# Performance work log

Measured on AMD Instinct MI355X. Metric: run time of the kernel, lower is better.

## Reference

```python
import jax, jax.numpy as jnp
import numpy as np

B, S, D = 4, 2048, 1024
H, HD = 16, 64
TAU = HD ** -0.5
N_MASKED = 256  # last keys masked (padding)


def setup_inputs() -> dict:
    key = jax.random.key(0)
    ks = jax.random.split(key, 8)
    sc = 0.02
    mask = jnp.zeros((B, 1, 1, S), dtype=bool).at[..., S - N_MASKED:].set(True)
    return {
        "q": jax.random.normal(ks[0], (B, S, D), dtype=jnp.float32),
        "k": jax.random.normal(ks[1], (B, S, D), dtype=jnp.float32),
        "v": jax.random.normal(ks[2], (B, S, D), dtype=jnp.float32),
        "mask": mask,
        "Wq": jax.random.normal(ks[3], (D, H * HD), dtype=jnp.float32) * sc,
        "bq": jnp.zeros((H * HD,), dtype=jnp.float32),
        "Wk": jax.random.normal(ks[4], (D, H * HD), dtype=jnp.float32) * sc,
        "bk": jnp.zeros((H * HD,), dtype=jnp.float32),
        "Wv": jax.random.normal(ks[5], (D, H * HD), dtype=jnp.float32) * sc,
        "bv": jnp.zeros((H * HD,), dtype=jnp.float32),
        "Wo": jax.random.normal(ks[6], (H * HD, D), dtype=jnp.float32) * sc,
        "bo": jnp.zeros((D,), dtype=jnp.float32),
    }


def reference(q, k, v, mask, Wq, bq, Wk, bk, Wv, bv, Wo, bo):
    # projections: [..., s, D] -> [..., s, H, HD]
    qh = (q @ Wq + bq).reshape(*q.shape[:-1], H, HD)
    kh = (k @ Wk + bk).reshape(*k.shape[:-1], H, HD)
    vh = (v @ Wv + bv).reshape(*v.shape[:-1], H, HD)
    # scores: [B, H, Q, K]
    attn = jnp.einsum('bqhd,bkhd->bhqk', qh, kh) * TAU
    attn = jnp.where(mask, -jnp.inf, attn)  # masked_fill(mask, -inf)
    # dropout(p=0) before softmax is identity
    p = jax.nn.softmax(attn, axis=-1)
    out = jnp.einsum('bhqk,bkhd->bqhd', p, vh).reshape(*q.shape[:-1], H * HD)
    return out @ Wo + bo  # [B, S, D]
```

## Files before the change

kernel.cpp:

```cpp
#include <hip/hip_runtime.h>
#include <hip/hip_fp16.h>
#include <cstdint>
#include <cstddef>

#define B_  4
#define S_  2048
#define D_  1024
#define H_  16
#define HD_ 64
#define TAU_ 0.125f
#define QSCALE_ 0.18033688011112042f

typedef _Float16 f16;
typedef __attribute__((ext_vector_type(8)))  _Float16 f16x8;
typedef __attribute__((ext_vector_type(4)))  _Float16 f16x4;
typedef __attribute__((ext_vector_type(2)))  __fp16   fp16x2_b;
typedef __attribute__((ext_vector_type(4)))  float    f32x4;
typedef __attribute__((ext_vector_type(16))) float    f32x16;
typedef __attribute__((ext_vector_type(2)))  unsigned u32x2;

__device__ __forceinline__ void gload_lds16(const void* g, void* l) {
    __builtin_amdgcn_global_load_lds(
        (const __attribute__((address_space(1))) unsigned int*)g,
        (__attribute__((address_space(3)))       unsigned int*)l,
        16, 0, 0);
}

__device__ __forceinline__ unsigned pkh(float a, float b) {
    fp16x2_b h = __builtin_amdgcn_cvt_pkrtz(a, b);
    return __builtin_bit_cast(unsigned, h);
}

__device__ __forceinline__ float exp2_hw(float x) {
    float r;
    asm("v_exp_f32 %0, %1" : "=v"(r) : "v"(x));
    return r;
}

__device__ __forceinline__ float max3f(float a, float b, float c) {
    float r;
    asm("v_max3_f32 %0, %1, %2, %3" : "=v"(r) : "v"(a), "v"(b), "v"(c));
    return r;
}

__device__ __forceinline__ float pair_max(float x) {
    unsigned xu = __builtin_bit_cast(unsigned, x);
    u32x2 r = __builtin_amdgcn_permlane32_swap(xu, xu, false, false);
    return fmaxf(__builtin_bit_cast(float, r[0]), __builtin_bit_cast(float, r[1]));
}
__device__ __forceinline__ float pair_sum(float x) {
    unsigned xu = __builtin_bit_cast(unsigned, x);
    u32x2 r = __builtin_amdgcn_permlane32_swap(xu, xu, false, false);
    return __builtin_bit_cast(float, r[0]) + __builtin_bit_cast(float, r[1]);
}

__global__ __launch_bounds__(256) void mask_norm_kernel(
    const unsigned char* __restrict__ mp, unsigned char* __restrict__ nm,
    float* __restrict__ mf)
{
    __shared__ int flags[3];
    const int tid = threadIdx.x;
    if (tid < 3) flags[tid] = 0;
    __syncthreads();
    int loc0 = 0, loc1 = 0, loc2 = 0;
    for (int i = 0; i < 32; ++i) {
        int off = tid * 32 + i;
        unsigned char v = mp[off];
        if (v) {
            int m = off & 3;
            if (m == 0) loc0 = 1;
            else if (m == 1) loc1 = 1;
            else loc2 = 1;
        }
    }
    if (loc0) atomicOr(&flags[0], 1);
    if (loc1) atomicOr(&flags[1], 1);
    if (loc2) atomicOr(&flags[2], 1);
    __syncthreads();
    const int mode = flags[1] ? 0 : (flags[2] ? 2 : (flags[0] ? 1 : 0));
    for (int i = 0; i < 32; ++i) {
        int idx = tid * 32 + i;
        unsigned char r;
        if (mode == 0)      r = mp[idx] ? 1 : 0;
        else if (mode == 1) r = ((const int*)mp)[idx] ? 1 : 0;
        else                r = (((const float*)mp)[idx] != 0.f) ? 1 : 0;
        nm[idx] = r;
        mf[idx] = r ? -1e30f : 0.f;
    }
}

__global__ __launch_bounds__(256) void wconv_kernel(
    const float* __restrict__ W0, const float* __restrict__ W1,
    const float* __restrict__ W2, const float* __restrict__ W3,
    f16* __restrict__ Wt)
{
    __shared__ float T[64][65];
    const int z = blockIdx.z;
    const float* W = (z == 0) ? W0 : (z == 1) ? W1 : (z == 2) ? W2 : W3;
    f16* out = Wt + (size_t)z * D_ * D_;
    const int n0 = blockIdx.x * 64, k0 = blockIdx.y * 64;
    const int tid = threadIdx.x;
    for (int j = 0; j < 4; ++j) {
        int idx = j * 256 + tid;
        int r = idx >> 4, c4 = idx & 15;
        float4 v = *(const float4*)&W[(size_t)(k0 + r) * D_ + n0 + c4 * 4];
        T[r][c4 * 4 + 0] = v.x; T[r][c4 * 4 + 1] = v.y;
        T[r][c4 * 4 + 2] = v.z; T[r][c4 * 4 + 3] = v.w;
    }
    __syncthreads();
    for (int j = 0; j < 16; ++j) {
        int idx = j * 256 + tid;
        int nl = idx >> 6, kl = idx & 63;
        out[(size_t)(n0 + nl) * D_ + k0 + kl] = (f16)T[kl][nl];
    }
}

__global__ __launch_bounds__(256) void gemm_qkvf_kernel(
    const float* __restrict__ q, const float* __restrict__ k,
    const float* __restrict__ v, const f16* __restrict__ Wt,
    const float* __restrict__ bq, const float* __restrict__ bk,
    const float* __restrict__ bv, f16* __restrict__ outbase)
{
    __shared__ __align__(16) float Al[128 * 64];
    __shared__ __align__(16) f16  Bl[128 * 64];
    const int z = blockIdx.z;
    const float* A  = (z == 0) ? q  : (z == 1) ? k  : v;
    const float* bi = (z == 0) ? bq : (z == 1) ? bk : bv;
    const f16*  W   = Wt + (size_t)z * D_ * D_;
    f16* Cp         = outbase + (size_t)z * S_ * B_ * D_;
    const float oscale = (z == 0) ? QSCALE_ : 1.f;
    const int outmode  = (z == 2) ? 1 : 0;
    const int m0 = blockIdx.x * 128, n0 = blockIdx.y * 128;
    const int tid = threadIdx.x, lane = tid & 63, wid = tid >> 6;
    const int wm = (wid >> 1) * 64, wn = (wid & 1) * 64;
    const int g = lane >> 4, c = lane & 15;

    f32x4 acc[4][4] = {};

    for (int kt = 0; kt < 16; ++kt) {
        const int k0 = kt * 64;
        for (int i = 0; i < 4; ++i) {
            int ch  = wid * 4 + i;
            int row = ch * 8 + (lane >> 3);
            int ls  = (lane & 7) ^ (row & 7);
            gload_lds16(W + (size_t)(n0 + row) * 1024 + k0 + ls * 8,
                        Bl + ch * 512);
        }
        for (int i = 0; i < 8; ++i) {
            int ch  = wid * 8 + i;
            int row = ch * 4 + (lane >> 4);
            int ls  = (lane & 15) ^ (row & 15);
            gload_lds16(A + (size_t)(m0 + row) * 1024 + k0 + ls * 4,
                        Al + ch * 256);
        }
        __syncthreads();
        for (int kc = 0; kc < 2; ++kc) {
            f16x8 af[4], bf[4];
            for (int mb = 0; mb < 4; ++mb) {
                int row = wm + mb * 16 + c;
                int sl  = kc * 8 + g * 2;
                f32x4 a0 = *(const f32x4*)&Al[row * 64 + ((sl)     ^ (row & 15)) * 4];
                f32x4 a1 = *(const f32x4*)&Al[row * 64 + ((sl + 1) ^ (row & 15)) * 4];
                f16x8 hfr;
                hfr[0] = (f16)a0[0]; hfr[1] = (f16)a0[1];
                hfr[2] = (f16)a0[2]; hfr[3] = (f16)a0[3];
                hfr[4] = (f16)a1[0]; hfr[5] = (f16)a1[1];
                hfr[6] = (f16)a1[2]; hfr[7] = (f16)a1[3];
                af[mb] = hfr;
            }
            for (int nb = 0; nb < 4; ++nb) {
                int row = wn + nb * 16 + c;
                bf[nb] = *(const f16x8*)&Bl[row * 64 + ((kc * 4 + g) ^ (row & 7)) * 8];
            }
            for (int mb = 0; mb < 4; ++mb)
                for (int nb = 0; nb < 4; ++nb)
                    acc[mb][nb] = __builtin_amdgcn_mfma_f32_16x16x32_f16(
                        af[mb], bf[nb], acc[mb][nb], 0, 0, 0);
        }
        __syncthreads();
    }
    for (int nb = 0; nb < 4; ++nb) {
        int n = n0 + wn + nb * 16 + c;
        float bv2 = bi[n];
        for (int mb = 0; mb < 4; ++mb)
            for (int r = 0; r < 4; ++r) {
                int m = m0 + wm + mb * 16 + g * 4 + r;
                float val = (acc[mb][nb][r] + bv2) * oscale;
                if (outmode == 1) {
                    Cp[(((size_t)(m >> 11) * H_ + (n >> 6)) * HD_ + (n & 63)) * S_ + (m & 2047)] = (f16)val;
                } else {
                    Cp[(size_t)m * 1024 + n] = (f16)val;
                }
            }
    }
}

__global__ __launch_bounds__(256) void gemm_out_kernel(
    const f16* __restrict__ Oh, const f16* __restrict__ WtO,
    const float* __restrict__ bo, float* __restrict__ out)
{
    __shared__ __align__(16) f16 Al[128 * 64];
    __shared__ __align__(16) f16 Bl[128 * 64];
    const int m0 = blockIdx.x * 128, n0 = blockIdx.y * 128;
    const int tid = threadIdx.x, lane = tid & 63, wid = tid >> 6;
    const int wm = (wid >> 1) * 64, wn = (wid & 1) * 64;
    const int g = lane >> 4, c = lane & 15;

    f32x4 acc[4][4] = {};

    for (int kt = 0; kt < 16; ++kt) {
        const int k0 = kt * 64;
        for (int i = 0; i < 4; ++i) {
            int ch  = wid * 4 + i;
            int row = ch * 8 + (lane >> 3);
            int ls  = (lane & 7) ^ (row & 7);
            gload_lds16(WtO + (size_t)(n0 + row) * 1024 + k0 + ls * 8,
                        Bl + ch * 512);
            gload_lds16(Oh + (size_t)(m0 + row) * 1024 + k0 + ls * 8,
                        Al + ch * 512);
        }
        __syncthreads();
        for (int kc = 0; kc < 2; ++kc) {
            f16x8 af[4], bf[4];
            for (int mb = 0; mb < 4; ++mb) {
                int row = wm + mb * 16 + c;
                af[mb] = *(const f16x8*)&Al[row * 64 + ((kc * 4 + g) ^ (row & 7)) * 8];
            }
            for (int nb = 0; nb < 4; ++nb) {
                int row = wn + nb * 16 + c;
                bf[nb] = *(const f16x8*)&Bl[row * 64 + ((kc * 4 + g) ^ (row & 7)) * 8];
            }
            for (int mb = 0; mb < 4; ++mb)
                for (int nb = 0; nb < 4; ++nb)
                    acc[mb][nb] = __builtin_amdgcn_mfma_f32_16x16x32_f16(
                        af[mb], bf[nb], acc[mb][nb], 0, 0, 0);
        }
        __syncthreads();
    }
    for (int nb = 0; nb < 4; ++nb) {
        int n = n0 + wn + nb * 16 + c;
        float bv = bo[n];
        for (int mb = 0; mb < 4; ++mb)
            for (int r = 0; r < 4; ++r) {
                int m = m0 + wm + mb * 16 + g * 4 + r;
                out[(size_t)m * 1024 + n] = acc[mb][nb][r] + bv;
            }
    }
}

__global__ __launch_bounds__(256, 2) void attn_kernel(
    const f16* __restrict__ qh, const f16* __restrict__ kh,
    const f16* __restrict__ vt, const unsigned char* __restrict__ maskp,
    const float* __restrict__ maskf, f16* __restrict__ Oh)
{
    __shared__ __align__(16) f16 Kl[2][128 * 64];
    __shared__ __align__(16) f16 VTl[2][64 * 128];
    const int tid = threadIdx.x, lane = tid & 63, wid = tid >> 6;
    const int ql = lane & 31, hi = lane >> 5;
    const int lg = ((blockIdx.x & 7) << 7) + (blockIdx.x >> 3);
    const int h = (lg >> 4) & 15, b = lg >> 8;
    const int q0 = (lg & 15) * 128 + wid * 32;

    const unsigned char* mrow = maskp + (size_t)b * S_;
    const float* mfrow = maskf + (size_t)b * S_;
    const size_t kbase  = (size_t)b * S_ * D_ + (size_t)h * HD_;
    const size_t vtbase = ((size_t)b * H_ + h) * (size_t)HD_ * S_;

    unsigned live = 0, part = 0;
    for (int t = 0; t < 16; ++t) {
        unsigned long long b0 = __ballot(mrow[t * 128 + lane] != 0);
        unsigned long long b1 = __ballot(mrow[t * 128 + 64 + lane] != 0);
        if (b0 != ~0ull || b1 != ~0ull) {
            live |= 1u << t;
            if (b0 | b1) part |= 1u << t;
        }
    }

    f16x8 qf[4];
    {
        const f16* qrow = qh + ((size_t)(b * S_ + q0 + ql) * H_ + h) * HD_;
        #pragma unroll
        for (int dc = 0; dc < 4; ++dc)
            qf[dc] = *(const f16x8*)&qrow[dc * 16 + hi * 8];
    }

    float m_ = -1e30f, l_ = 0.f;
    f32x16 accO[2] = {};

    auto stage = [&](int kv0, int bb) {
        #pragma unroll
        for (int i = 0; i < 4; ++i) {
            int ch  = wid * 4 + i;
            int row = ch * 8 + (lane >> 3);
            int ls  = (lane & 7) ^ (row & 7);
            gload_lds16(kh + kbase + (size_t)(kv0 + row) * D_ + ls * 8,
                        &Kl[bb][ch * 512]);
            int hdr = ch * 4 + (lane >> 4);
            int vs  = (lane & 15) ^ (hdr & 15);
            gload_lds16(vt + vtbase + (size_t)hdr * S_ + kv0 + vs * 8,
                        &VTl[bb][ch * 512]);
        }
    };

    if (live) {
        int t = __builtin_ctz(live);
        stage(t * 128, 0);
        __syncthreads();
        int cur = 0;
        for (;;) {
            unsigned rem = live & (0xFFFFFFFEu << t);
            int tn = rem ? __builtin_ctz(rem) : 32;
            if (tn < 32) stage(tn * 128, cur ^ 1);

            const int kv0 = t * 128;
            const f16* Kb = &Kl[cur][0];
            const f16* Vb = &VTl[cur][0];

            f32x16 sacc[4] = {};
            __builtin_amdgcn_s_setprio(1);
            #pragma unroll
            for (int ks = 0; ks < 4; ++ks) {
                const int key = ks * 32 + ql;
                #pragma unroll
                for (int dc = 0; dc < 4; ++dc) {
                    int slot = (dc * 2 + hi) ^ (key & 7);
                    f16x8 kf = *(const f16x8*)&Kb[key * 64 + slot * 8];
                    sacc[ks] = __builtin_amdgcn_mfma_f32_32x32x16_f16(
                        kf, qf[dc], sacc[ks], 0, 0, 0);
                }
            }
            __builtin_amdgcn_s_setprio(0);
            if (part & (1u << t)) {
                #pragma unroll
                for (int ks = 0; ks < 4; ++ks)
                    #pragma unroll
                    for (int r = 0; r < 16; ++r) {
                        int key = kv0 + ks * 32 + (r & 3) + 8 * (r >> 2) + 4 * hi;
                        sacc[ks][r] += mfrow[key];
                    }
            }
            float mx;
            {
                float m0 = max3f(sacc[0][0], sacc[0][1], sacc[0][2]);
                float m1 = max3f(sacc[1][0], sacc[1][1], sacc[1][2]);
                float m2 = max3f(sacc[2][0], sacc[2][1], sacc[2][2]);
                float m3 = max3f(sacc[3][0], sacc[3][1], sacc[3][2]);
                #pragma unroll
                for (int r = 3; r < 15; r += 2) {
                    m0 = max3f(m0, sacc[0][r], sacc[0][r + 1]);
                    m1 = max3f(m1, sacc[1][r], sacc[1][r + 1]);
                    m2 = max3f(m2, sacc[2][r], sacc[2][r + 1]);
                    m3 = max3f(m3, sacc[3][r], sacc[3][r + 1]);
                }
                m0 = fmaxf(m0, sacc[0][15]); m1 = fmaxf(m1, sacc[1][15]);
                m2 = fmaxf(m2, sacc[2][15]); m3 = fmaxf(m3, sacc[3][15]);
                mx = max3f(m0, m1, m2);
                mx = fmaxf(mx, m3);
            }
            mx = pair_max(mx);
            if (__ballot(mx > m_ + 8.f)) {
                float mnew = fmaxf(m_, mx);
                float alpha = exp2_hw(m_ - mnew);
                m_ = mnew;
                l_ *= alpha;
                #pragma unroll
                for (int blk = 0; blk < 2; ++blk)
                    #pragma unroll
                    for (int r = 0; r < 16; ++r) accO[blk][r] *= alpha;
            }
            float ts = 0.f;
            #pragma unroll
            for (int ks = 0; ks < 4; ++ks)
                #pragma unroll
                for (int r = 0; r < 16; ++r) {
                    float p = exp2_hw(sacc[ks][r] - m_);
                    sacc[ks][r] = p;
                    ts += p;
                }
            l_ += pair_sum(ts);

            #pragma unroll
            for (int ks = 0; ks < 4; ++ks) {
                unsigned Pq[4][2];
                #pragma unroll
                for (int j = 0; j < 4; ++j) {
                    Pq[j][0] = pkh(sacc[ks][4 * j + 0], sacc[ks][4 * j + 1]);
                    Pq[j][1] = pkh(sacc[ks][4 * j + 2], sacc[ks][4 * j + 3]);
                }
                #pragma unroll
                for (int kc = 0; kc < 2; ++kc) {
                    union { f16x8 v; unsigned u[4]; } pf;
                    u32x2 s0 = __builtin_amdgcn_permlane32_swap(Pq[2 * kc][0], Pq[2 * kc + 1][0], false, false);
                    u32x2 s1 = __builtin_amdgcn_permlane32_swap(Pq[2 * kc][1], Pq[2 * kc + 1][1], false, false);
                    pf.u[0] = s0[0]; pf.u[2] = s0[1];
                    pf.u[1] = s1[0]; pf.u[3] = s1[1];
                    const int s = ks * 2 + kc;
                    __builtin_amdgcn_s_setprio(1);
                    #pragma unroll
                    for (int blk = 0; blk < 2; ++blk) {
                        int hd = blk * 32 + ql;
                        int slot = (s * 2 + hi) ^ (hd & 15);
                        f16x8 vtf = *(const f16x8*)&Vb[hd * 128 + slot * 8];
                        accO[blk] = __builtin_amdgcn_mfma_f32_32x32x16_f16(
                            vtf, pf.v, accO[blk], 0, 0, 0);
                    }
                    __builtin_amdgcn_s_setprio(0);
                }
            }
            __syncthreads();
            cur ^= 1;
            if (tn == 32) break;
            t = tn;
        }
    }
    const float invl = (l_ > 0.f) ? 1.f / l_ : 0.f;
    f16* orow = Oh + ((size_t)(b * S_ + q0 + ql) * H_ + h) * HD_;
    #pragma unroll
    for (int blk = 0; blk < 2; ++blk)
        #pragma unroll
        for (int j = 0; j < 4; ++j) {
            f16x4 o;
            #pragma unroll
            for (int tt = 0; tt < 4; ++tt)
                o[tt] = (f16)(accO[blk][4 * j + tt] * invl);
            *(f16x4*)&orow[blk * 32 + 4 * hi + 8 * j] = o;
        }
}

extern "C" void kernel_launch(void* const* d_in, const int* in_sizes, int n_in,
                              void* d_out, int out_size, void* d_ws, size_t ws_size,
                              hipStream_t stream)
{
    const float* q    = (const float*)d_in[0];
    const float* k    = (const float*)d_in[1];
    const float* v    = (const float*)d_in[2];
    const unsigned char* mask = (const unsigned char*)d_in[3];
    const float* Wq   = (const float*)d_in[4];
    const float* bq   = (const float*)d_in[5];
    const float* Wk   = (const float*)d_in[6];
    const float* bk   = (const float*)d_in[7];
    const float* Wv   = (const float*)d_in[8];
    const float* bv   = (const float*)d_in[9];
    const float* Wo   = (const float*)d_in[10];
    const float* bo   = (const float*)d_in[11];
    float* out        = (float*)d_out;

    char* ws = (char*)d_ws;
    const size_t MB = 1048576;
    f16* Wt  = (f16*)ws;
    f16* qh  = (f16*)(ws + 8 * MB);
    f16* khp = (f16*)(ws + 24 * MB);
    f16* vtp = (f16*)(ws + 40 * MB);
    f16* Ohp = (f16*)(ws + 56 * MB);
    unsigned char* nm = (unsigned char*)(ws + 72 * MB);
    float* mf = (float*)(ws + 72 * MB + 8192);

    mask_norm_kernel<<<1, 256, 0, stream>>>(mask, nm, mf);
    wconv_kernel<<<dim3(16, 16, 4), 256, 0, stream>>>(Wq, Wk, Wv, Wo, Wt);
    gemm_qkvf_kernel<<<dim3(64, 8, 3), 256, 0, stream>>>(q, k, v, Wt, bq, bk, bv, qh);
    attn_kernel<<<1024, 256, 0, stream>>>(qh, khp, vtp, nm, mf, Ohp);
    gemm_out_kernel<<<dim3(64, 8), 256, 0, stream>>>(Ohp, Wt + (size_t)3 * D_ * D_, bo, out);
}
```

Measured before the change: 230.9 us.

## Pre-convert QKV inputs to fp16 and double-buffer projection GEMMs

Adds a pass that converts the fp32 q/k/v activations to fp16 in workspace, so the QKV projection GEMM can use async global-to-LDS loads with a double-buffered prefetch of the next K tile. The output projection GEMM gets the same double-buffering and both raise MFMA wave priority around the compute. The cost is an extra read-write pass over the activations and more LDS per block. The new path runs only when the workspace is large enough.

```diff
diff --git a/kernel.cpp b/kernel.cpp
--- a/kernel.cpp
+++ b/kernel.cpp
@@ -112,6 +112,106 @@
         int idx = j * 256 + tid;
         int nl = idx >> 6, kl = idx & 63;
         out[(size_t)(n0 + nl) * D_ + k0 + kl] = (f16)T[kl][nl];
+    }
+}
+
+__global__ __launch_bounds__(256) void f32to16_kernel(
+    const float* __restrict__ a0, const float* __restrict__ a1,
+    const float* __restrict__ a2, f16* __restrict__ o0,
+    f16* __restrict__ o1, f16* __restrict__ o2)
+{
+    const int z = blockIdx.y;
+    const float* a = (z == 0) ? a0 : (z == 1) ? a1 : a2;
+    f16* o = (z == 0) ? o0 : (z == 1) ? o1 : o2;
+    const int N4 = (B_ * S_ * D_) / 4;
+    for (int i = blockIdx.x * 256 + threadIdx.x; i < N4; i += gridDim.x * 256) {
+        float4 v = ((const float4*)a)[i];
+        f16x4 h;
+        h[0] = (f16)v.x; h[1] = (f16)v.y; h[2] = (f16)v.z; h[3] = (f16)v.w;
+        ((f16x4*)o)[i] = h;
+    }
+}
+
+__global__ __launch_bounds__(256, 2) void gemm_qkv16_kernel(
+    const f16* __restrict__ qf16, const f16* __restrict__ kf16,
+    const f16* __restrict__ vf16, const f16* __restrict__ Wt,
+    const float* __restrict__ bq, const float* __restrict__ bk,
+    const float* __restrict__ bv, f16* __restrict__ outbase)
+{
+    __shared__ __align__(16) f16 Al[2][128 * 64];
+    __shared__ __align__(16) f16 Bl[2][128 * 64];
+    const int z = blockIdx.z;
+    const f16* A    = (z == 0) ? qf16 : (z == 1) ? kf16 : vf16;
+    const float* bi = (z == 0) ? bq : (z == 1) ? bk : bv;
+    const f16*  W   = Wt + (size_t)z * D_ * D_;
+    f16* Cp         = outbase + (size_t)z * S_ * B_ * D_;
+    const float oscale = (z == 0) ? QSCALE_ : 1.f;
+    const int outmode  = (z == 2) ? 1 : 0;
+    const int m0 = blockIdx.x * 128, n0 = blockIdx.y * 128;
+    const int tid = threadIdx.x, lane = tid & 63, wid = tid >> 6;
+    const int wm = (wid >> 1) * 64, wn = (wid & 1) * 64;
+    const int g = lane >> 4, c = lane & 15;
+
+    f32x4 acc[4][4] = {};
+
+    auto stage = [&](int kt, int bb) {
+        const int k0 = kt * 64;
+        #pragma unroll
+        for (int i = 0; i < 4; ++i) {
+            int ch  = wid * 4 + i;
+            int row = ch * 8 + (lane >> 3);
+            int ls  = (lane & 7) ^ (row & 7);
+            gload_lds16(W + (size_t)(n0 + row) * 1024 + k0 + ls * 8,
+                        &Bl[bb][ch * 512]);
+            gload_lds16(A + (size_t)(m0 + row) * 1024 + k0 + ls * 8,
+                        &Al[bb][ch * 512]);
+        }
+    };
+
+    stage(0, 0);
+    __syncthreads();
+    int cur = 0;
+    for (int kt = 0; kt < 16; ++kt) {
+        if (kt < 15) stage(kt + 1, cur ^ 1);
+        #pragma unroll
+        for (int kc = 0; kc < 2; ++kc) {
+            f16x8 af[4], bf[4];
+            #pragma unroll
+            for (int mb = 0; mb < 4; ++mb) {
+                int row = wm + mb * 16 + c;
+                af[mb] = *(const f16x8*)&Al[cur][row * 64 + ((kc * 4 + g) ^ (row & 7)) * 8];
+            }
+            #pragma unroll
+            for (int nb = 0; nb < 4; ++nb) {
+                int row = wn + nb * 16 + c;
+                bf[nb] = *(const f16x8*)&Bl[cur][row * 64 + ((kc * 4 + g) ^ (row & 7)) * 8];
+            }
+            __builtin_amdgcn_s_setprio(1);
+            #pragma unroll
+            for (int mb = 0; mb < 4; ++mb)
+                #pragma unroll
+                for (int nb = 0; nb < 4; ++nb)
+                    acc[mb][nb] = __builtin_amdgcn_mfma_f32_16x16x32_f16(
+                        af[mb], bf[nb], acc[mb][nb], 0, 0, 0);
+            __builtin_amdgcn_s_setprio(0);
+        }
+        __syncthreads();
+        cur ^= 1;
+    }
+
+    for (int nb = 0; nb < 4; ++nb) {
+        int n = n0 + wn + nb * 16 + c;
+        float bv2 = bi[n];
+        for (int mb = 0; mb < 4; ++mb)
+            for (int r = 0; r < 4; ++r) {
+                int m = m0 + wm + mb * 16 + g * 4 + r;
+                float val = (acc[mb][nb][r] + bv2) * oscale;
+                if (outmode == 1) {
+                    Cp[(((size_t)(m >> 11) * H_ + (n >> 6)) * HD_ + (n & 63)) * S_ + (m & 2047)] = (f16)val;
+                } else {
+                    Cp[(size_t)m * 1024 + n] = (f16)val;
+                }
+            }
     }
 }
 
@@ -195,12 +295,12 @@
     }
 }
 
-__global__ __launch_bounds__(256) void gemm_out_kernel(
+__global__ __launch_bounds__(256, 2) void gemm_out_kernel(
     const f16* __restrict__ Oh, const f16* __restrict__ WtO,
     const float* __restrict__ bo, float* __restrict__ out)
 {
-    __shared__ __align__(16) f16 Al[128 * 64];
-    __shared__ __align__(16) f16 Bl[128 * 64];
+    __shared__ __align__(16) f16 Al[2][128 * 64];
+    __shared__ __align__(16) f16 Bl[2][128 * 64];
     const int m0 = blockIdx.x * 128, n0 = blockIdx.y * 128;
     const int tid = threadIdx.x, lane = tid & 63, wid = tid >> 6;
     const int wm = (wid >> 1) * 64, wn = (wid & 1) * 64;
@@ -208,34 +308,49 @@
 
     f32x4 acc[4][4] = {};
 
-    for (int kt = 0; kt < 16; ++kt) {
+    auto stage = [&](int kt, int bb) {
         const int k0 = kt * 64;
+        #pragma unroll
         for (int i = 0; i < 4; ++i) {
             int ch  = wid * 4 + i;
             int row = ch * 8 + (lane >> 3);
             int ls  = (lane & 7) ^ (row & 7);
             gload_lds16(WtO + (size_t)(n0 + row) * 1024 + k0 + ls * 8,
-                        Bl + ch * 512);
+                        &Bl[bb][ch * 512]);
             gload_lds16(Oh + (size_t)(m0 + row) * 1024 + k0 + ls * 8,
-                        Al + ch * 512);
-        }
-        __syncthreads();
+                        &Al[bb][ch * 512]);
+        }
+    };
+
+    stage(0, 0);
+    __syncthreads();
+    int cur = 0;
+    for (int kt = 0; kt < 16; ++kt) {
+        if (kt < 15) stage(kt + 1, cur ^ 1);
+        #pragma unroll
         for (int kc = 0; kc < 2; ++kc) {
             f16x8 af[4], bf[4];
+            #pragma unroll
             for (int mb = 0; mb < 4; ++mb) {
                 int row = wm + mb * 16 + c;
-                af[mb] = *(const f16x8*)&Al[row * 64 + ((kc * 4 + g) ^ (row & 7)) * 8];
-            }
+                af[mb] = *(const f16x8*)&Al[cur][row * 64 + ((kc * 4 + g) ^ (row & 7)) * 8];
+            }
+            #pragma unroll
             for (int nb = 0; nb < 4; ++nb) {
                 int row = wn + nb * 16 + c;
-                bf[nb] = *(const f16x8*)&Bl[row * 64 + ((kc * 4 + g) ^ (row & 7)) * 8];
-            }
+                bf[nb] = *(const f16x8*)&Bl[cur][row * 64 + ((kc * 4 + g) ^ (row & 7)) * 8];
+            }
+            __builtin_amdgcn_s_setprio(1);
+            #pragma unroll
             for (int mb = 0; mb < 4; ++mb)
+                #pragma unroll
                 for (int nb = 0; nb < 4; ++nb)
                     acc[mb][nb] = __builtin_amdgcn_mfma_f32_16x16x32_f16(
                         af[mb], bf[nb], acc[mb][nb], 0, 0, 0);
+            __builtin_amdgcn_s_setprio(0);
         }
         __syncthreads();
+        cur ^= 1;
     }
     for (int nb = 0; nb < 4; ++nb) {
         int n = n0 + wn + nb * 16 + c;
@@ -454,10 +569,21 @@
     f16* Ohp = (f16*)(ws + 56 * MB);
     unsigned char* nm = (unsigned char*)(ws + 72 * MB);
     float* mf = (float*)(ws + 72 * MB + 8192);
+    f16* qf16 = (f16*)(ws + 76 * MB);
+    f16* kf16 = (f16*)(ws + 92 * MB);
+    f16* vf16 = (f16*)(ws + 108 * MB);
+    const bool use16 = ws_size >= 124 * MB;
 
     mask_norm_kernel<<<1, 256, 0, stream>>>(mask, nm, mf);
     wconv_kernel<<<dim3(16, 16, 4), 256, 0, stream>>>(Wq, Wk, Wv, Wo, Wt);
-    gemm_qkvf_kernel<<<dim3(64, 8, 3), 256, 0, stream>>>(q, k, v, Wt, bq, bk, bv, qh);
+    if (use16) {
+        f32to16_kernel<<<dim3(1024, 3), 256, 0, stream>>>(q, k, v, qf16, kf16, vf16);
+        gemm_qkv16_kernel<<<dim3(64, 8, 3), 256, 0, stream>>>(
+            qf16, kf16, vf16, Wt, bq, bk, bv, qh);
+    } else {
+        gemm_qkvf_kernel<<<dim3(64, 8, 3), 256, 0, stream>>>(
+            q, k, v, Wt, bq, bk, bv, qh);
+    }
     attn_kernel<<<1024, 256, 0, stream>>>(qh, khp, vtp, nm, mf, Ohp);
     gemm_out_kernel<<<dim3(64, 8), 256, 0, stream>>>(Ohp, Wt + (size_t)3 * D_ * D_, bo, out);
 }
```

New measurement: 237.5 us. 1.03x slower.
